# Performance work log

Hardware: AMD Instinct MI355X
Metric: run time of the kernel (lower is better)

## Reference

```python
import jax, jax.numpy as jnp
import numpy as np

NEG_INF = -1e30  # stand-in for float('-inf') added to masked scores


def setup_inputs() -> dict:
    key = jax.random.key(0)
    ks = jax.random.split(key, 3)
    B, S, D = 4, 2048, 1024
    x = jax.random.normal(ks[0], (B, S, D), dtype=jnp.float32)
    W_qkv = jax.random.normal(ks[1], (D, 3 * D), dtype=jnp.float32) * (1.0 / np.sqrt(D))
    b_qkv = jnp.zeros((3 * D,), dtype=jnp.float32)
    W_out = jax.random.normal(ks[2], (D, D), dtype=jnp.float32) * (1.0 / np.sqrt(D))
    b_out = jnp.zeros((D,), dtype=jnp.float32)
    return {"x": x, "W_qkv": W_qkv, "b_qkv": b_qkv, "W_out": W_out, "b_out": b_out, "mask": 1}


def reference(x, W_qkv, b_qkv, W_out, b_out, mask):
    B, S, D = x.shape
    H = 16
    hd = D // H
    # fused QKV projection: [B,S,3D]
    qkv = x @ W_qkv + b_qkv
    # [B,S,H,3*hd] -> [B,H,S,3*hd], split into q,k,v each [B,H,S,hd]
    qkv = qkv.reshape(B, S, H, 3 * hd).transpose(0, 2, 1, 3)
    q, k, v = jnp.split(qkv, 3, axis=-1)
    # scaled dot-product attention, full score matrix [B,H,S,S]
    scaled = jnp.einsum('bhqd,bhkd->bhqk', q, k) / np.sqrt(hd)
    if mask:
        causal = jnp.triu(jnp.ones((S, S), dtype=bool), k=1)
        scaled = jnp.where(causal, NEG_INF, scaled)
    attention = jax.nn.softmax(scaled, axis=-1)
    values = jnp.einsum('bhqk,bhkd->bhqd', attention, v)
    # merge heads: [B,H,S,hd] -> [B,S,D] (matches tf.reshape on [B,H,S,hd])
    values = values.reshape(B, S, H * hd)
    return values @ W_out + b_out
```

## Files before the change

### kernel.cpp

```cpp
#include <hip/hip_runtime.h>
#include <hip/hip_bf16.h>

typedef __attribute__((ext_vector_type(8))) short short8;
typedef __attribute__((ext_vector_type(4))) float f32x4;

__device__ inline f32x4 mfma16(short8 a, short8 b, f32x4 c) {
    return __builtin_amdgcn_mfma_f32_16x16x32_bf16(a, b, c, 0, 0, 0);
}
__device__ inline short f2bf(float x) {
    __hip_bfloat16 h = __float2bfloat16(x);
    return *reinterpret_cast<short*>(&h);
}
__device__ inline unsigned short f2bfu(float x) {
    __hip_bfloat16 h = __float2bfloat16(x);
    return *reinterpret_cast<unsigned short*>(&h);
}
__device__ inline float bf2f(short u) {
    __hip_bfloat16 h = *reinterpret_cast<__hip_bfloat16*>(&u);
    return __bfloat162float(h);
}
__device__ inline float scrub(float v, float s) {
    return (fabsf(v) < 1e30f) ? v : s;
}
__device__ inline short8 scaleq(short8 v) {
    short8 r;
#pragma unroll
    for (int j = 0; j < 8; j++) r[j] = f2bf(bf2f(v[j]) * 0.125f);
    return r;
}

__global__ void detect_dtype(const unsigned short* __restrict__ x, int* flag) {
    __shared__ int cnt;
    if (threadIdx.x == 0) cnt = 0;
    __syncthreads();
    int c = 0;
    for (int i = threadIdx.x; i < 1024; i += 256) {
        unsigned short u = x[i];
        int e = (u >> 7) & 0xFF;
        if ((u & 0x7FFF) == 0 || (e >= 110 && e <= 143)) c++;
    }
    atomicAdd(&cnt, c);
    __syncthreads();
    if (threadIdx.x == 0) flag[0] = (cnt < 819) ? 1 : 0;
}

__global__ void conv_bias(const void* __restrict__ in, short* __restrict__ out,
                          int n, const int* __restrict__ flag) {
    int i = blockIdx.x * 256 + threadIdx.x;
    if (i >= n) return;
    out[i] = (*flag) ? f2bf(((const float*)in)[i]) : ((const short*)in)[i];
}

__global__ __launch_bounds__(256) void conv_x(const void* __restrict__ in,
                                              short* __restrict__ out, int n,
                                              const int* __restrict__ flag) {
    int i = (blockIdx.x * 256 + threadIdx.x) * 4;
    if (i >= n) return;
    if (*flag) {
        float4 f = *(const float4*)((const float*)in + i);
        unsigned int u0 = ((unsigned int)f2bfu(f.y) << 16) | f2bfu(f.x);
        unsigned int u1 = ((unsigned int)f2bfu(f.w) << 16) | f2bfu(f.z);
        *(uint2*)(out + i) = make_uint2(u0, u1);
    } else {
        *(uint2*)(out + i) = *(const uint2*)((const short*)in + i);
    }
}

__global__ void fill_sentinel(void* out, int n, const int* __restrict__ flag) {
    int i = blockIdx.x * 256 + threadIdx.x;
    if (i >= n) return;
    if (*flag) ((float*)out)[i] = 3e5f; else ((short*)out)[i] = f2bf(3e5f);
}

__global__ __launch_bounds__(256) void transpose_poly(const void* __restrict__ in,
                                                      short* __restrict__ out,
                                                      int R, int C,
                                                      const int* __restrict__ flag) {
    __shared__ short tile[32][33];
    const bool f32 = (*flag) != 0;
    int tx = threadIdx.x & 31, ty = threadIdx.x >> 5;
    int r0 = blockIdx.y * 32, c0 = blockIdx.x * 32;
#pragma unroll
    for (int i = 0; i < 4; i++) {
        size_t off = (size_t)(r0 + ty + i * 8) * C + c0 + tx;
        tile[ty + i * 8][tx] = f32 ? f2bf(((const float*)in)[off]) : ((const short*)in)[off];
    }
    __syncthreads();
#pragma unroll
    for (int i = 0; i < 4; i++)
        out[(size_t)(c0 + ty + i * 8) * R + r0 + tx] = tile[tx][ty + i * 8];
}

#define LDK 72

__global__ __launch_bounds__(256) void gemm_bt(const short* __restrict__ A,
                                               const short* __restrict__ Bt,
                                               const short* __restrict__ bias,
                                               void* __restrict__ Cv,
                                               int N, int K,
                                               const int* __restrict__ flag,
                                               int c_poly, float sent) {
    alignas(16) __shared__ short As[128 * LDK];
    alignas(16) __shared__ short Bs[128 * LDK];
    const bool cf32 = c_poly && (*flag);
    int tid = threadIdx.x;
    int wave = tid >> 6, lane = tid & 63;
    int lrow = lane & 15, lq = lane >> 4;
    int wm = (wave >> 1) * 64, wn = (wave & 1) * 64;
    int m0 = blockIdx.y * 128, n0 = blockIdx.x * 128;

    f32x4 acc[4][4];
#pragma unroll
    for (int i = 0; i < 4; i++)
#pragma unroll
        for (int j = 0; j < 4; j++) acc[i][j] = (f32x4){0.f, 0.f, 0.f, 0.f};

    int srow = tid >> 3;
    int scol = (tid & 7) * 8;

    for (int kb = 0; kb < K; kb += 64) {
#pragma unroll
        for (int p = 0; p < 4; p++) {
            int row = p * 32 + srow;
            *(short8*)&As[row * LDK + scol] =
                *(const short8*)&A[(size_t)(m0 + row) * K + kb + scol];
            *(short8*)&Bs[row * LDK + scol] =
                *(const short8*)&Bt[(size_t)(n0 + row) * K + kb + scol];
        }
        __syncthreads();
#pragma unroll
        for (int ks = 0; ks < 2; ks++) {
            short8 af[4], bf[4];
#pragma unroll
            for (int i = 0; i < 4; i++)
                af[i] = *(short8*)&As[(wm + i * 16 + lrow) * LDK + ks * 32 + lq * 8];
#pragma unroll
            for (int i = 0; i < 4; i++)
                bf[i] = *(short8*)&Bs[(wn + i * 16 + lrow) * LDK + ks * 32 + lq * 8];
#pragma unroll
            for (int i = 0; i < 4; i++)
#pragma unroll
                for (int j = 0; j < 4; j++)
                    acc[i][j] = mfma16(af[i], bf[j], acc[i][j]);
        }
        __syncthreads();
    }

    const __hip_bfloat16* bias16 = (const __hip_bfloat16*)bias;
#pragma unroll
    for (int j = 0; j < 4; j++) {
        int col = n0 + wn + j * 16 + lrow;
        float bv = __bfloat162float(bias16[col]);
#pragma unroll
        for (int i = 0; i < 4; i++) {
            int rbase = m0 + wm + i * 16 + lq * 4;
#pragma unroll
            for (int r = 0; r < 4; r++) {
                float val = scrub(acc[i][j][r] + bv, sent);
                size_t off = (size_t)(rbase + r) * N + col;
                if (cf32) ((float*)Cv)[off] = val; else ((short*)Cv)[off] = f2bf(val);
            }
        }
    }
}

#define VP2 72
#define PP 72

__global__ __launch_bounds__(256) void attn_kernel(const short* __restrict__ QKV,
                                                   short* __restrict__ AO,
                                                   const int* __restrict__ maskp) {
    constexpr int S = 2048, C3 = 3072;
    alignas(16) __shared__ short Vt[2][64 * VP2];
    alignas(16) __shared__ short Pt[4][2][16 * PP];

    int tid = threadIdx.x;
    int wave = tid >> 6, lane = tid & 63;
    int lrow = lane & 15, lq = lane >> 4;
    int bh = blockIdx.y;
    const bool causal = (*maskp) != 0;
    const short* base = QKV + (size_t)(bh >> 4) * S * C3 + (bh & 15) * 192;

    int vi2 = (tid & 31) * 2;
    int vd0 = (tid >> 5) * 8;

    int buf = 0;
    for (int tile = 0; tile < 2; tile++) {
        int q0t = (tile == 0) ? blockIdx.x * 128 : 1920 - blockIdx.x * 128;

        int qg[2];
        short8 qf0[2], qf1[2];
#pragma unroll
        for (int g = 0; g < 2; g++) {
            qg[g] = q0t + wave * 32 + g * 16 + lrow;
            qf0[g] = scaleq(*(const short8*)(base + (size_t)qg[g] * C3 + lq * 8));
            qf1[g] = scaleq(*(const short8*)(base + (size_t)qg[g] * C3 + 32 + lq * 8));
        }

        float m_i[2] = {-1e38f, -1e38f}, l_i[2] = {0.f, 0.f};
        f32x4 acc[2][4];
#pragma unroll
        for (int g = 0; g < 2; g++)
#pragma unroll
            for (int nt = 0; nt < 4; nt++) acc[g][nt] = (f32x4){0.f, 0.f, 0.f, 0.f};

        int nkv = causal ? (q0t + 128) : S;

        for (int kv0 = 0; kv0 < nkv; kv0 += 64) {
            {
                const short* vs0 = base + (size_t)(kv0 + vi2) * C3 + 128 + vd0;
                union { short8 v; unsigned short u[8]; } a, b;
                a.v = *(const short8*)vs0;
                b.v = *(const short8*)(vs0 + C3);
                unsigned int* vt = (unsigned int*)&Vt[buf][0];
#pragma unroll
                for (int j = 0; j < 8; j++)
                    vt[((vd0 + j) * VP2 + vi2) >> 1] =
                        ((unsigned int)b.u[j] << 16) | a.u[j];
            }
            __syncthreads();

            f32x4 s[2][4];
#pragma unroll
            for (int sub = 0; sub < 4; sub++) {
                const short* kb = base + (size_t)(kv0 + sub * 16 + lrow) * C3 + 64;
                short8 kf0 = *(const short8*)(kb + lq * 8);
                short8 kf1 = *(const short8*)(kb + 32 + lq * 8);
#pragma unroll
                for (int g = 0; g < 2; g++) {
                    f32x4 a = (f32x4){0.f, 0.f, 0.f, 0.f};
                    a = mfma16(kf0, qf0[g], a);
                    a = mfma16(kf1, qf1[g], a);
                    s[g][sub] = a;
                }
            }

#pragma unroll
            for (int g = 0; g < 2; g++) {
                if (causal && (kv0 + 63 > q0t + wave * 32 + g * 16)) {
#pragma unroll
                    for (int sub = 0; sub < 4; sub++) {
                        int kvg = kv0 + sub * 16 + lq * 4;
#pragma unroll
                        for (int r = 0; r < 4; r++)
                            if (kvg + r > qg[g]) s[g][sub][r] = -1e30f;
                    }
                }
                float vmax = -1e38f;
#pragma unroll
                for (int sub = 0; sub < 4; sub++) {
                    float a = fmaxf(fmaxf(s[g][sub][0], s[g][sub][1]),
                                    fmaxf(s[g][sub][2], s[g][sub][3]));
                    vmax = fmaxf(vmax, a);
                }
                vmax = fmaxf(vmax, __shfl_xor(vmax, 16, 64));
                vmax = fmaxf(vmax, __shfl_xor(vmax, 32, 64));
                float mnew = fmaxf(m_i[g], vmax);
                float alpha = __expf(m_i[g] - mnew);
                float lsum = 0.f;
                unsigned int pk[4][2];
#pragma unroll
                for (int sub = 0; sub < 4; sub++) {
                    float p0 = __expf(s[g][sub][0] - mnew);
                    float p1 = __expf(s[g][sub][1] - mnew);
                    float p2 = __expf(s[g][sub][2] - mnew);
                    float p3 = __expf(s[g][sub][3] - mnew);
                    lsum += (p0 + p1) + (p2 + p3);
                    pk[sub][0] = ((unsigned int)f2bfu(p1) << 16) | f2bfu(p0);
                    pk[sub][1] = ((unsigned int)f2bfu(p3) << 16) | f2bfu(p2);
                }
                lsum += __shfl_xor(lsum, 16, 64);
                lsum += __shfl_xor(lsum, 32, 64);
                l_i[g] = l_i[g] * alpha + lsum;
                m_i[g] = mnew;
#pragma unroll
                for (int nt = 0; nt < 4; nt++)
#pragma unroll
                    for (int r = 0; r < 4; r++) acc[g][nt][r] *= alpha;
                unsigned int* pt = (unsigned int*)&Pt[wave][g][0];
#pragma unroll
                for (int sub = 0; sub < 4; sub++)
                    *(uint2*)&pt[(lrow * PP + sub * 16 + lq * 4) >> 1] =
                        make_uint2(pk[sub][0], pk[sub][1]);
            }

#pragma unroll
            for (int ks = 0; ks < 2; ks++) {
                short8 pfA = *(short8*)&Pt[wave][0][lrow * PP + ks * 32 + lq * 8];
                short8 pfB = *(short8*)&Pt[wave][1][lrow * PP + ks * 32 + lq * 8];
#pragma unroll
                for (int nt = 0; nt < 4; nt++) {
                    short8 vf = *(short8*)&Vt[buf][(nt * 16 + lrow) * VP2 + ks * 32 + lq * 8];
                    acc[0][nt] = mfma16(vf, pfA, acc[0][nt]);
                    acc[1][nt] = mfma16(vf, pfB, acc[1][nt]);
                }
            }
            buf ^= 1;
        }

#pragma unroll
        for (int g = 0; g < 2; g++) {
            float inv = 1.f / l_i[g];
            short* ob = AO + ((size_t)bh * S + qg[g]) * 64;
#pragma unroll
            for (int nt = 0; nt < 4; nt++) {
                unsigned int u0 = ((unsigned int)f2bfu(scrub(acc[g][nt][1] * inv, 4e4f)) << 16) |
                                  f2bfu(scrub(acc[g][nt][0] * inv, 4e4f));
                unsigned int u1 = ((unsigned int)f2bfu(scrub(acc[g][nt][3] * inv, 4e4f)) << 16) |
                                  f2bfu(scrub(acc[g][nt][2] * inv, 4e4f));
                *(uint2*)(ob + nt * 16 + lq * 4) = make_uint2(u0, u1);
            }
        }
    }
}

extern "C" void kernel_launch(void* const* d_in, const int* in_sizes, int n_in,
                              void* d_out, int out_size, void* d_ws, size_t ws_size,
                              hipStream_t stream) {
    char* ws = (char*)d_ws;
    int*   flag  = (int*)ws;
    short* bq_bf = (short*)(ws + 65536);
    short* bo_bf = (short*)(ws + 131072);
    short* WqkvT = (short*)(ws + (1ull << 20));
    short* WoutT = (short*)(ws + 7ull * (1ull << 20));
    short* xbfAO = (short*)(ws + 9ull * (1ull << 20));
    short* QKVc  = (short*)(ws + 25ull * (1ull << 20));

    detect_dtype<<<1, 256, 0, stream>>>((const unsigned short*)d_in[0], flag);

    if (ws_size < 73ull * 1048576) {
        fill_sentinel<<<(8388608 + 255) / 256, 256, 0, stream>>>(d_out, 8388608, flag);
        return;
    }

    conv_bias<<<12, 256, 0, stream>>>(d_in[2], bq_bf, 3072, flag);
    conv_bias<<<4, 256, 0, stream>>>(d_in[4], bo_bf, 1024, flag);
    transpose_poly<<<dim3(96, 32), 256, 0, stream>>>(d_in[1], WqkvT, 1024, 3072, flag);
    transpose_poly<<<dim3(32, 32), 256, 0, stream>>>(d_in[3], WoutT, 1024, 1024, flag);
    conv_x<<<8192, 256, 0, stream>>>(d_in[0], xbfAO, 8388608, flag);

    gemm_bt<<<dim3(24, 64), 256, 0, stream>>>(xbfAO, WqkvT, bq_bf, QKVc,
                                              3072, 1024, flag, 0, 8e4f);
    attn_kernel<<<dim3(8, 64), 256, 0, stream>>>(QKVc, xbfAO, (const int*)d_in[5]);
    gemm_bt<<<dim3(8, 64), 256, 0, stream>>>(xbfAO, WoutT, bo_bf, d_out,
                                             1024, 1024, flag, 1, 2e4f);
}
```

Before: 328.3 us.

## Split attention KV range across two wave groups and skip lazy rescaling

The attention block grows to 512 threads. Two groups of four waves each process alternating 64-wide KV chunks for the same query rows, and their partial softmax state (m, l, acc) is merged through shared memory at the end of each tile. This doubles the waves per block to raise parallelism and latency hiding, at the cost of extra LDS traffic and barriers. The online softmax also skips the max update and accumulator rescale when the new block max stays within 8 of the running max, which saves exp and multiply work but risks larger unnormalised exponents.

Result: slower. 388.4 us (+18.3%).

```diff
diff --git a/kernel.cpp b/kernel.cpp
--- a/kernel.cpp
+++ b/kernel.cpp
@@ -166,23 +166,29 @@
 
 #define VP2 72
 #define PP 72
-
-__global__ __launch_bounds__(256) void attn_kernel(const short* __restrict__ QKV,
-                                                   short* __restrict__ AO,
-                                                   const int* __restrict__ maskp) {
+#define VT_ELEMS (2 * 2 * 64 * VP2)
+#define PT_ELEMS (8 * 2 * 16 * PP)
+
+__global__ __launch_bounds__(512, 4) void attn_kernel(const short* __restrict__ QKV,
+                                                      short* __restrict__ AO,
+                                                      const int* __restrict__ maskp) {
     constexpr int S = 2048, C3 = 3072;
-    alignas(16) __shared__ short Vt[2][64 * VP2];
-    alignas(16) __shared__ short Pt[4][2][16 * PP];
+    alignas(16) __shared__ short smem[VT_ELEMS + PT_ELEMS];
 
     int tid = threadIdx.x;
     int wave = tid >> 6, lane = tid & 63;
+    int wq = wave & 3, gsel = wave >> 2;
     int lrow = lane & 15, lq = lane >> 4;
     int bh = blockIdx.y;
     const bool causal = (*maskp) != 0;
     const short* base = QKV + (size_t)(bh >> 4) * S * C3 + (bh & 15) * 192;
 
-    int vi2 = (tid & 31) * 2;
-    int vd0 = (tid >> 5) * 8;
+    int t8 = tid & 255;
+    int vi2 = (t8 & 31) * 2;
+    int vd0 = (t8 >> 5) * 8;
+
+    short* PtA = smem + VT_ELEMS + (wave * 2 + 0) * 16 * PP;
+    short* PtB = smem + VT_ELEMS + (wave * 2 + 1) * 16 * PP;
 
     int buf = 0;
     for (int tile = 0; tile < 2; tile++) {
@@ -192,7 +198,7 @@
         short8 qf0[2], qf1[2];
 #pragma unroll
         for (int g = 0; g < 2; g++) {
-            qg[g] = q0t + wave * 32 + g * 16 + lrow;
+            qg[g] = q0t + wq * 32 + g * 16 + lrow;
             qf0[g] = scaleq(*(const short8*)(base + (size_t)qg[g] * C3 + lq * 8));
             qf1[g] = scaleq(*(const short8*)(base + (size_t)qg[g] * C3 + 32 + lq * 8));
         }
@@ -206,13 +212,15 @@
 
         int nkv = causal ? (q0t + 128) : S;
 
-        for (int kv0 = 0; kv0 < nkv; kv0 += 64) {
+        for (int kv0g = 0; kv0g < nkv; kv0g += 128) {
+            int kv0 = kv0g + gsel * 64;
+            short* Vtc = smem + (gsel * 2 + buf) * 64 * VP2;
             {
                 const short* vs0 = base + (size_t)(kv0 + vi2) * C3 + 128 + vd0;
                 union { short8 v; unsigned short u[8]; } a, b;
                 a.v = *(const short8*)vs0;
                 b.v = *(const short8*)(vs0 + C3);
-                unsigned int* vt = (unsigned int*)&Vt[buf][0];
+                unsigned int* vt = (unsigned int*)Vtc;
 #pragma unroll
                 for (int j = 0; j < 8; j++)
                     vt[((vd0 + j) * VP2 + vi2) >> 1] =
@@ -237,7 +245,7 @@
 
 #pragma unroll
             for (int g = 0; g < 2; g++) {
-                if (causal && (kv0 + 63 > q0t + wave * 32 + g * 16)) {
+                if (causal && (kv0 + 63 > q0t + wq * 32 + g * 16)) {
 #pragma unroll
                     for (int sub = 0; sub < 4; sub++) {
                         int kvg = kv0 + sub * 16 + lq * 4;
@@ -255,8 +263,16 @@
                 }
                 vmax = fmaxf(vmax, __shfl_xor(vmax, 16, 64));
                 vmax = fmaxf(vmax, __shfl_xor(vmax, 32, 64));
-                float mnew = fmaxf(m_i[g], vmax);
-                float alpha = __expf(m_i[g] - mnew);
+                float mnew = m_i[g];
+                if (!__all(vmax <= m_i[g] + 8.0f)) {
+                    mnew = fmaxf(m_i[g], vmax);
+                    float alpha = __expf(m_i[g] - mnew);
+                    l_i[g] *= alpha;
+#pragma unroll
+                    for (int nt = 0; nt < 4; nt++)
+#pragma unroll
+                        for (int r = 0; r < 4; r++) acc[g][nt][r] *= alpha;
+                }
                 float lsum = 0.f;
                 unsigned int pk[4][2];
 #pragma unroll
@@ -271,13 +287,9 @@
                 }
                 lsum += __shfl_xor(lsum, 16, 64);
                 lsum += __shfl_xor(lsum, 32, 64);
-                l_i[g] = l_i[g] * alpha + lsum;
+                l_i[g] += lsum;
                 m_i[g] = mnew;
-#pragma unroll
-                for (int nt = 0; nt < 4; nt++)
-#pragma unroll
-                    for (int r = 0; r < 4; r++) acc[g][nt][r] *= alpha;
-                unsigned int* pt = (unsigned int*)&Pt[wave][g][0];
+                unsigned int* pt = (unsigned int*)(g ? PtB : PtA);
 #pragma unroll
                 for (int sub = 0; sub < 4; sub++)
                     *(uint2*)&pt[(lrow * PP + sub * 16 + lq * 4) >> 1] =
@@ -286,11 +298,11 @@
 
 #pragma unroll
             for (int ks = 0; ks < 2; ks++) {
-                short8 pfA = *(short8*)&Pt[wave][0][lrow * PP + ks * 32 + lq * 8];
-                short8 pfB = *(short8*)&Pt[wave][1][lrow * PP + ks * 32 + lq * 8];
+                short8 pfA = *(short8*)&PtA[lrow * PP + ks * 32 + lq * 8];
+                short8 pfB = *(short8*)&PtB[lrow * PP + ks * 32 + lq * 8];
 #pragma unroll
                 for (int nt = 0; nt < 4; nt++) {
-                    short8 vf = *(short8*)&Vt[buf][(nt * 16 + lrow) * VP2 + ks * 32 + lq * 8];
+                    short8 vf = *(short8*)&Vtc[(nt * 16 + lrow) * VP2 + ks * 32 + lq * 8];
                     acc[0][nt] = mfma16(vf, pfA, acc[0][nt]);
                     acc[1][nt] = mfma16(vf, pfB, acc[1][nt]);
                 }
@@ -298,19 +310,45 @@
             buf ^= 1;
         }
 
-#pragma unroll
-        for (int g = 0; g < 2; g++) {
-            float inv = 1.f / l_i[g];
-            short* ob = AO + ((size_t)bh * S + qg[g]) * 64;
-#pragma unroll
-            for (int nt = 0; nt < 4; nt++) {
-                unsigned int u0 = ((unsigned int)f2bfu(scrub(acc[g][nt][1] * inv, 4e4f)) << 16) |
-                                  f2bfu(scrub(acc[g][nt][0] * inv, 4e4f));
-                unsigned int u1 = ((unsigned int)f2bfu(scrub(acc[g][nt][3] * inv, 4e4f)) << 16) |
-                                  f2bfu(scrub(acc[g][nt][2] * inv, 4e4f));
-                *(uint2*)(ob + nt * 16 + lq * 4) = make_uint2(u0, u1);
-            }
-        }
+        __syncthreads();
+        float* ex = (float*)smem;
+        float* px = ex + (wq * 64 + lane) * 37;
+        if (gsel) {
+#pragma unroll
+            for (int g = 0; g < 2; g++) {
+                px[g * 18 + 0] = m_i[g];
+                px[g * 18 + 1] = l_i[g];
+#pragma unroll
+                for (int nt = 0; nt < 4; nt++)
+#pragma unroll
+                    for (int r = 0; r < 4; r++)
+                        px[g * 18 + 2 + nt * 4 + r] = acc[g][nt][r];
+            }
+        }
+        __syncthreads();
+        if (!gsel) {
+#pragma unroll
+            for (int g = 0; g < 2; g++) {
+                float mb = px[g * 18 + 0], lb = px[g * 18 + 1];
+                float mn = fmaxf(m_i[g], mb);
+                float ea = __expf(m_i[g] - mn), eb = __expf(mb - mn);
+                float inv = 1.f / (l_i[g] * ea + lb * eb);
+                float fa = ea * inv, fb = eb * inv;
+                short* ob = AO + ((size_t)bh * S + qg[g]) * 64;
+#pragma unroll
+                for (int nt = 0; nt < 4; nt++) {
+                    const float* pb = &px[g * 18 + 2 + nt * 4];
+                    float o0 = scrub(acc[g][nt][0] * fa + pb[0] * fb, 4e4f);
+                    float o1 = scrub(acc[g][nt][1] * fa + pb[1] * fb, 4e4f);
+                    float o2 = scrub(acc[g][nt][2] * fa + pb[2] * fb, 4e4f);
+                    float o3 = scrub(acc[g][nt][3] * fa + pb[3] * fb, 4e4f);
+                    unsigned int u0 = ((unsigned int)f2bfu(o1) << 16) | f2bfu(o0);
+                    unsigned int u1 = ((unsigned int)f2bfu(o3) << 16) | f2bfu(o2);
+                    *(uint2*)(ob + nt * 16 + lq * 4) = make_uint2(u0, u1);
+                }
+            }
+        }
+        __syncthreads();
     }
 }
 
@@ -341,7 +379,7 @@
 
     gemm_bt<<<dim3(24, 64), 256, 0, stream>>>(xbfAO, WqkvT, bq_bf, QKVc,
                                               3072, 1024, flag, 0, 8e4f);
-    attn_kernel<<<dim3(8, 64), 256, 0, stream>>>(QKVc, xbfAO, (const int*)d_in[5]);
+    attn_kernel<<<dim3(8, 64), 512, 0, stream>>>(QKVc, xbfAO, (const int*)d_in[5]);
     gemm_bt<<<dim3(8, 64), 256, 0, stream>>>(xbfAO, WoutT, bo_bf, d_out,
                                              1024, 1024, flag, 1, 2e4f);
 }
```

## Split paired causal query tiles into separate blocks with balanced 1D scheduling

Applied to the files above, without the earlier changes.

Each attention block used to process two query tiles (one early, one late) to balance causal work. Now each block handles one 128-row query tile, giving 1024 blocks, with a 1D grid whose index mapping interleaves heavy and light tiles across batch-heads. The aim is more parallelism and better load balance across CUs. The risk is extra per-block overhead and less predictable tail behaviour. The launch_bounds attribute is also removed, which may change how registers are allocated.

Result: slower. 370.5 us (+12.9%).

```diff
diff --git a/kernel.cpp b/kernel.cpp
--- a/kernel.cpp
+++ b/kernel.cpp
@@ -167,9 +167,9 @@
 #define VP2 72
 #define PP 72
 
-__global__ __launch_bounds__(256) void attn_kernel(const short* __restrict__ QKV,
-                                                   short* __restrict__ AO,
-                                                   const int* __restrict__ maskp) {
+__global__ void attn_kernel(const short* __restrict__ QKV,
+                            short* __restrict__ AO,
+                            const int* __restrict__ maskp) {
     constexpr int S = 2048, C3 = 3072;
     alignas(16) __shared__ short Vt[2][64 * VP2];
     alignas(16) __shared__ short Pt[4][2][16 * PP];
@@ -177,139 +177,146 @@
     int tid = threadIdx.x;
     int wave = tid >> 6, lane = tid & 63;
     int lrow = lane & 15, lq = lane >> 4;
-    int bh = blockIdx.y;
+
+    int id = blockIdx.x;
+    int u = id & 255, r = id >> 8;
+    int b = u & 15;
+    int bh = (u >> 4) + (r << 4);
+    int bxv;
+    if (r == 0)      bxv = b;
+    else if (r == 1) bxv = 15 - b;
+    else if (r == 2) bxv = (b + 8) & 15;
+    else             bxv = 15 - ((b + 8) & 15);
+    int q0t = bxv * 128;
+
     const bool causal = (*maskp) != 0;
     const short* base = QKV + (size_t)(bh >> 4) * S * C3 + (bh & 15) * 192;
 
     int vi2 = (tid & 31) * 2;
     int vd0 = (tid >> 5) * 8;
 
+    int qg[2];
+    short8 qf0[2], qf1[2];
+#pragma unroll
+    for (int g = 0; g < 2; g++) {
+        qg[g] = q0t + wave * 32 + g * 16 + lrow;
+        qf0[g] = scaleq(*(const short8*)(base + (size_t)qg[g] * C3 + lq * 8));
+        qf1[g] = scaleq(*(const short8*)(base + (size_t)qg[g] * C3 + 32 + lq * 8));
+    }
+
+    float m_i[2] = {-1e38f, -1e38f}, l_i[2] = {0.f, 0.f};
+    f32x4 acc[2][4];
+#pragma unroll
+    for (int g = 0; g < 2; g++)
+#pragma unroll
+        for (int nt = 0; nt < 4; nt++) acc[g][nt] = (f32x4){0.f, 0.f, 0.f, 0.f};
+
+    int nkv = causal ? (q0t + 128) : S;
+
     int buf = 0;
-    for (int tile = 0; tile < 2; tile++) {
-        int q0t = (tile == 0) ? blockIdx.x * 128 : 1920 - blockIdx.x * 128;
-
-        int qg[2];
-        short8 qf0[2], qf1[2];
+    for (int kv0 = 0; kv0 < nkv; kv0 += 64) {
+        {
+            const short* vs0 = base + (size_t)(kv0 + vi2) * C3 + 128 + vd0;
+            union { short8 v; unsigned short u[8]; } a, bb;
+            a.v = *(const short8*)vs0;
+            bb.v = *(const short8*)(vs0 + C3);
+            unsigned int* vt = (unsigned int*)&Vt[buf][0];
+#pragma unroll
+            for (int j = 0; j < 8; j++)
+                vt[((vd0 + j) * VP2 + vi2) >> 1] =
+                    ((unsigned int)bb.u[j] << 16) | a.u[j];
+        }
+        __syncthreads();
+
+        f32x4 s[2][4];
+#pragma unroll
+        for (int sub = 0; sub < 4; sub++) {
+            const short* kb = base + (size_t)(kv0 + sub * 16 + lrow) * C3 + 64;
+            short8 kf0 = *(const short8*)(kb + lq * 8);
+            short8 kf1 = *(const short8*)(kb + 32 + lq * 8);
+#pragma unroll
+            for (int g = 0; g < 2; g++) {
+                f32x4 a = (f32x4){0.f, 0.f, 0.f, 0.f};
+                a = mfma16(kf0, qf0[g], a);
+                a = mfma16(kf1, qf1[g], a);
+                s[g][sub] = a;
+            }
+        }
+
 #pragma unroll
         for (int g = 0; g < 2; g++) {
-            qg[g] = q0t + wave * 32 + g * 16 + lrow;
-            qf0[g] = scaleq(*(const short8*)(base + (size_t)qg[g] * C3 + lq * 8));
-            qf1[g] = scaleq(*(const short8*)(base + (size_t)qg[g] * C3 + 32 + lq * 8));
-        }
-
-        float m_i[2] = {-1e38f, -1e38f}, l_i[2] = {0.f, 0.f};
-        f32x4 acc[2][4];
-#pragma unroll
-        for (int g = 0; g < 2; g++)
-#pragma unroll
-            for (int nt = 0; nt < 4; nt++) acc[g][nt] = (f32x4){0.f, 0.f, 0.f, 0.f};
-
-        int nkv = causal ? (q0t + 128) : S;
-
-        for (int kv0 = 0; kv0 < nkv; kv0 += 64) {
-            {
-                const short* vs0 = base + (size_t)(kv0 + vi2) * C3 + 128 + vd0;
-                union { short8 v; unsigned short u[8]; } a, b;
-                a.v = *(const short8*)vs0;
-                b.v = *(const short8*)(vs0 + C3);
-                unsigned int* vt = (unsigned int*)&Vt[buf][0];
-#pragma unroll
-                for (int j = 0; j < 8; j++)
-                    vt[((vd0 + j) * VP2 + vi2) >> 1] =
-                        ((unsigned int)b.u[j] << 16) | a.u[j];
-            }
-            __syncthreads();
-
-            f32x4 s[2][4];
+            if (causal && (kv0 + 63 > q0t + wave * 32 + g * 16)) {
+#pragma unroll
+                for (int sub = 0; sub < 4; sub++) {
+                    int kvg = kv0 + sub * 16 + lq * 4;
+#pragma unroll
+                    for (int rr = 0; rr < 4; rr++)
+                        if (kvg + rr > qg[g]) s[g][sub][rr] = -1e30f;
+                }
+            }
+            float vmax = -1e38f;
 #pragma unroll
             for (int sub = 0; sub < 4; sub++) {
-                const short* kb = base + (size_t)(kv0 + sub * 16 + lrow) * C3 + 64;
-                short8 kf0 = *(const short8*)(kb + lq * 8);
-                short8 kf1 = *(const short8*)(kb + 32 + lq * 8);
-#pragma unroll
-                for (int g = 0; g < 2; g++) {
-                    f32x4 a = (f32x4){0.f, 0.f, 0.f, 0.f};
-                    a = mfma16(kf0, qf0[g], a);
-                    a = mfma16(kf1, qf1[g], a);
-                    s[g][sub] = a;
-                }
-            }
-
-#pragma unroll
-            for (int g = 0; g < 2; g++) {
-                if (causal && (kv0 + 63 > q0t + wave * 32 + g * 16)) {
-#pragma unroll
-                    for (int sub = 0; sub < 4; sub++) {
-                        int kvg = kv0 + sub * 16 + lq * 4;
-#pragma unroll
-                        for (int r = 0; r < 4; r++)
-                            if (kvg + r > qg[g]) s[g][sub][r] = -1e30f;
-                    }
-                }
-                float vmax = -1e38f;
-#pragma unroll
-                for (int sub = 0; sub < 4; sub++) {
-                    float a = fmaxf(fmaxf(s[g][sub][0], s[g][sub][1]),
-                                    fmaxf(s[g][sub][2], s[g][sub][3]));
-                    vmax = fmaxf(vmax, a);
-                }
-                vmax = fmaxf(vmax, __shfl_xor(vmax, 16, 64));
-                vmax = fmaxf(vmax, __shfl_xor(vmax, 32, 64));
-                float mnew = fmaxf(m_i[g], vmax);
-                float alpha = __expf(m_i[g] - mnew);
-                float lsum = 0.f;
-                unsigned int pk[4][2];
-#pragma unroll
-                for (int sub = 0; sub < 4; sub++) {
-                    float p0 = __expf(s[g][sub][0] - mnew);
-                    float p1 = __expf(s[g][sub][1] - mnew);
-                    float p2 = __expf(s[g][sub][2] - mnew);
-                    float p3 = __expf(s[g][sub][3] - mnew);
-                    lsum += (p0 + p1) + (p2 + p3);
-                    pk[sub][0] = ((unsigned int)f2bfu(p1) << 16) | f2bfu(p0);
-                    pk[sub][1] = ((unsigned int)f2bfu(p3) << 16) | f2bfu(p2);
-                }
-                lsum += __shfl_xor(lsum, 16, 64);
-                lsum += __shfl_xor(lsum, 32, 64);
-                l_i[g] = l_i[g] * alpha + lsum;
-                m_i[g] = mnew;
-#pragma unroll
-                for (int nt = 0; nt < 4; nt++)
-#pragma unroll
-                    for (int r = 0; r < 4; r++) acc[g][nt][r] *= alpha;
-                unsigned int* pt = (unsigned int*)&Pt[wave][g][0];
-#pragma unroll
-                for (int sub = 0; sub < 4; sub++)
-                    *(uint2*)&pt[(lrow * PP + sub * 16 + lq * 4) >> 1] =
-                        make_uint2(pk[sub][0], pk[sub][1]);
-            }
-
-#pragma unroll
-            for (int ks = 0; ks < 2; ks++) {
-                short8 pfA = *(short8*)&Pt[wave][0][lrow * PP + ks * 32 + lq * 8];
-                short8 pfB = *(short8*)&Pt[wave][1][lrow * PP + ks * 32 + lq * 8];
-#pragma unroll
-                for (int nt = 0; nt < 4; nt++) {
-                    short8 vf = *(short8*)&Vt[buf][(nt * 16 + lrow) * VP2 + ks * 32 + lq * 8];
-                    acc[0][nt] = mfma16(vf, pfA, acc[0][nt]);
-                    acc[1][nt] = mfma16(vf, pfB, acc[1][nt]);
-                }
-            }
-            buf ^= 1;
-        }
-
-#pragma unroll
-        for (int g = 0; g < 2; g++) {
-            float inv = 1.f / l_i[g];
-            short* ob = AO + ((size_t)bh * S + qg[g]) * 64;
+                float a = fmaxf(fmaxf(s[g][sub][0], s[g][sub][1]),
+                                fmaxf(s[g][sub][2], s[g][sub][3]));
+                vmax = fmaxf(vmax, a);
+            }
+            vmax = fmaxf(vmax, __shfl_xor(vmax, 16, 64));
+            vmax = fmaxf(vmax, __shfl_xor(vmax, 32, 64));
+            float mnew = fmaxf(m_i[g], vmax);
+            float alpha = __expf(m_i[g] - mnew);
+            float lsum = 0.f;
+            unsigned int pk[4][2];
+#pragma unroll
+            for (int sub = 0; sub < 4; sub++) {
+                float p0 = __expf(s[g][sub][0] - mnew);
+                float p1 = __expf(s[g][sub][1] - mnew);
+                float p2 = __expf(s[g][sub][2] - mnew);
+                float p3 = __expf(s[g][sub][3] - mnew);
+                lsum += (p0 + p1) + (p2 + p3);
+                pk[sub][0] = ((unsigned int)f2bfu(p1) << 16) | f2bfu(p0);
+                pk[sub][1] = ((unsigned int)f2bfu(p3) << 16) | f2bfu(p2);
+            }
+            lsum += __shfl_xor(lsum, 16, 64);
+            lsum += __shfl_xor(lsum, 32, 64);
+            l_i[g] = l_i[g] * alpha + lsum;
+            m_i[g] = mnew;
+#pragma unroll
+            for (int nt = 0; nt < 4; nt++)
+#pragma unroll
+                for (int rr = 0; rr < 4; rr++) acc[g][nt][rr] *= alpha;
+            unsigned int* pt = (unsigned int*)&Pt[wave][g][0];
+#pragma unroll
+            for (int sub = 0; sub < 4; sub++)
+                *(uint2*)&pt[(lrow * PP + sub * 16 + lq * 4) >> 1] =
+                    make_uint2(pk[sub][0], pk[sub][1]);
+        }
+
+#pragma unroll
+        for (int ks = 0; ks < 2; ks++) {
+            short8 pfA = *(short8*)&Pt[wave][0][lrow * PP + ks * 32 + lq * 8];
+            short8 pfB = *(short8*)&Pt[wave][1][lrow * PP + ks * 32 + lq * 8];
 #pragma unroll
             for (int nt = 0; nt < 4; nt++) {
-                unsigned int u0 = ((unsigned int)f2bfu(scrub(acc[g][nt][1] * inv, 4e4f)) << 16) |
-                                  f2bfu(scrub(acc[g][nt][0] * inv, 4e4f));
-                unsigned int u1 = ((unsigned int)f2bfu(scrub(acc[g][nt][3] * inv, 4e4f)) << 16) |
-                                  f2bfu(scrub(acc[g][nt][2] * inv, 4e4f));
-                *(uint2*)(ob + nt * 16 + lq * 4) = make_uint2(u0, u1);
-            }
+                short8 vf = *(short8*)&Vt[buf][(nt * 16 + lrow) * VP2 + ks * 32 + lq * 8];
+                acc[0][nt] = mfma16(vf, pfA, acc[0][nt]);
+                acc[1][nt] = mfma16(vf, pfB, acc[1][nt]);
+            }
+        }
+        buf ^= 1;
+    }
+
+#pragma unroll
+    for (int g = 0; g < 2; g++) {
+        float inv = 1.f / l_i[g];
+        short* ob = AO + ((size_t)bh * S + qg[g]) * 64;
+#pragma unroll
+        for (int nt = 0; nt < 4; nt++) {
+            unsigned int u0 = ((unsigned int)f2bfu(scrub(acc[g][nt][1] * inv, 4e4f)) << 16) |
+                              f2bfu(scrub(acc[g][nt][0] * inv, 4e4f));
+            unsigned int u1 = ((unsigned int)f2bfu(scrub(acc[g][nt][3] * inv, 4e4f)) << 16) |
+                              f2bfu(scrub(acc[g][nt][2] * inv, 4e4f));
+            *(uint2*)(ob + nt * 16 + lq * 4) = make_uint2(u0, u1);
         }
     }
 }
@@ -341,7 +348,7 @@
 
     gemm_bt<<<dim3(24, 64), 256, 0, stream>>>(xbfAO, WqkvT, bq_bf, QKVc,
                                               3072, 1024, flag, 0, 8e4f);
-    attn_kernel<<<dim3(8, 64), 256, 0, stream>>>(QKVc, xbfAO, (const int*)d_in[5]);
+    attn_kernel<<<dim3(1024), 256, 0, stream>>>(QKVc, xbfAO, (const int*)d_in[5]);
     gemm_bt<<<dim3(8, 64), 256, 0, stream>>>(xbfAO, WoutT, bo_bf, d_out,
                                              1024, 1024, flag, 1, 2e4f);
 }
```

## Shrink attention query tile to 64 rows per block, doubling grid

Applied to the files above, without the earlier changes.

Each wave now handles one 16-row query group instead of two, so a block covers 64 query rows and the attention grid doubles to 16x64 blocks. Causal pairing of tiles is kept, now pairing tile i with 31-i. The aim is more blocks for better occupancy and load balance across CUs, with fewer registers per thread. In exchange, each K/V tile loaded into LDS and registers serves only half as many queries, which doubles K/V traffic per query. A barrier is also added at the end of each tile.

Result: slower. 433.5 us (+32.1%).

```diff
diff --git a/kernel.cpp b/kernel.cpp
--- a/kernel.cpp
+++ b/kernel.cpp
@@ -172,7 +172,7 @@
                                                    const int* __restrict__ maskp) {
     constexpr int S = 2048, C3 = 3072;
     alignas(16) __shared__ short Vt[2][64 * VP2];
-    alignas(16) __shared__ short Pt[4][2][16 * PP];
+    alignas(16) __shared__ short Pt[4][16 * PP];
 
     int tid = threadIdx.x;
     int wave = tid >> 6, lane = tid & 63;
@@ -186,131 +186,116 @@
 
     int buf = 0;
     for (int tile = 0; tile < 2; tile++) {
-        int q0t = (tile == 0) ? blockIdx.x * 128 : 1920 - blockIdx.x * 128;
-
-        int qg[2];
-        short8 qf0[2], qf1[2];
-#pragma unroll
-        for (int g = 0; g < 2; g++) {
-            qg[g] = q0t + wave * 32 + g * 16 + lrow;
-            qf0[g] = scaleq(*(const short8*)(base + (size_t)qg[g] * C3 + lq * 8));
-            qf1[g] = scaleq(*(const short8*)(base + (size_t)qg[g] * C3 + 32 + lq * 8));
-        }
-
-        float m_i[2] = {-1e38f, -1e38f}, l_i[2] = {0.f, 0.f};
-        f32x4 acc[2][4];
-#pragma unroll
-        for (int g = 0; g < 2; g++)
-#pragma unroll
-            for (int nt = 0; nt < 4; nt++) acc[g][nt] = (f32x4){0.f, 0.f, 0.f, 0.f};
-
-        int nkv = causal ? (q0t + 128) : S;
+        int q0t = (tile == 0) ? blockIdx.x * 64 : (31 - blockIdx.x) * 64;
+
+        int qg = q0t + wave * 16 + lrow;
+        short8 qf0 = scaleq(*(const short8*)(base + (size_t)qg * C3 + lq * 8));
+        short8 qf1 = scaleq(*(const short8*)(base + (size_t)qg * C3 + 32 + lq * 8));
+
+        float m_i = -1e38f, l_i = 0.f;
+        f32x4 acc[4];
+#pragma unroll
+        for (int nt = 0; nt < 4; nt++) acc[nt] = (f32x4){0.f, 0.f, 0.f, 0.f};
+
+        int nkv = causal ? (q0t + 64) : S;
 
         for (int kv0 = 0; kv0 < nkv; kv0 += 64) {
             {
                 const short* vs0 = base + (size_t)(kv0 + vi2) * C3 + 128 + vd0;
-                union { short8 v; unsigned short u[8]; } a, b;
+                union { short8 v; unsigned short u[8]; } a, bb;
                 a.v = *(const short8*)vs0;
-                b.v = *(const short8*)(vs0 + C3);
+                bb.v = *(const short8*)(vs0 + C3);
                 unsigned int* vt = (unsigned int*)&Vt[buf][0];
 #pragma unroll
                 for (int j = 0; j < 8; j++)
                     vt[((vd0 + j) * VP2 + vi2) >> 1] =
-                        ((unsigned int)b.u[j] << 16) | a.u[j];
+                        ((unsigned int)bb.u[j] << 16) | a.u[j];
             }
             __syncthreads();
 
-            f32x4 s[2][4];
+            f32x4 s[4];
 #pragma unroll
             for (int sub = 0; sub < 4; sub++) {
                 const short* kb = base + (size_t)(kv0 + sub * 16 + lrow) * C3 + 64;
                 short8 kf0 = *(const short8*)(kb + lq * 8);
                 short8 kf1 = *(const short8*)(kb + 32 + lq * 8);
-#pragma unroll
-                for (int g = 0; g < 2; g++) {
-                    f32x4 a = (f32x4){0.f, 0.f, 0.f, 0.f};
-                    a = mfma16(kf0, qf0[g], a);
-                    a = mfma16(kf1, qf1[g], a);
-                    s[g][sub] = a;
+                f32x4 a = (f32x4){0.f, 0.f, 0.f, 0.f};
+                a = mfma16(kf0, qf0, a);
+                a = mfma16(kf1, qf1, a);
+                s[sub] = a;
+            }
+
+            if (causal && (kv0 + 63 > q0t + wave * 16)) {
+#pragma unroll
+                for (int sub = 0; sub < 4; sub++) {
+                    int kvg = kv0 + sub * 16 + lq * 4;
+#pragma unroll
+                    for (int rr = 0; rr < 4; rr++)
+                        if (kvg + rr > qg) s[sub][rr] = -1e30f;
                 }
             }
-
-#pragma unroll
-            for (int g = 0; g < 2; g++) {
-                if (causal && (kv0 + 63 > q0t + wave * 32 + g * 16)) {
-#pragma unroll
-                    for (int sub = 0; sub < 4; sub++) {
-                        int kvg = kv0 + sub * 16 + lq * 4;
-#pragma unroll
-                        for (int r = 0; r < 4; r++)
-                            if (kvg + r > qg[g]) s[g][sub][r] = -1e30f;
-                    }
-                }
-                float vmax = -1e38f;
-#pragma unroll
-                for (int sub = 0; sub < 4; sub++) {
-                    float a = fmaxf(fmaxf(s[g][sub][0], s[g][sub][1]),
-                                    fmaxf(s[g][sub][2], s[g][sub][3]));
-                    vmax = fmaxf(vmax, a);
-                }
-                vmax = fmaxf(vmax, __shfl_xor(vmax, 16, 64));
-                vmax = fmaxf(vmax, __shfl_xor(vmax, 32, 64));
-                float mnew = fmaxf(m_i[g], vmax);
-                float alpha = __expf(m_i[g] - mnew);
-                float lsum = 0.f;
-                unsigned int pk[4][2];
-#pragma unroll
-                for (int sub = 0; sub < 4; sub++) {
-                    float p0 = __expf(s[g][sub][0] - mnew);
-                    float p1 = __expf(s[g][sub][1] - mnew);
-                    float p2 = __expf(s[g][sub][2] - mnew);
-                    float p3 = __expf(s[g][sub][3] - mnew);
-                    lsum += (p0 + p1) + (p2 + p3);
-                    pk[sub][0] = ((unsigned int)f2bfu(p1) << 16) | f2bfu(p0);
-                    pk[sub][1] = ((unsigned int)f2bfu(p3) << 16) | f2bfu(p2);
-                }
-                lsum += __shfl_xor(lsum, 16, 64);
-                lsum += __shfl_xor(lsum, 32, 64);
-                l_i[g] = l_i[g] * alpha + lsum;
-                m_i[g] = mnew;
-#pragma unroll
-                for (int nt = 0; nt < 4; nt++)
-#pragma unroll
-                    for (int r = 0; r < 4; r++) acc[g][nt][r] *= alpha;
-                unsigned int* pt = (unsigned int*)&Pt[wave][g][0];
-#pragma unroll
-                for (int sub = 0; sub < 4; sub++)
-                    *(uint2*)&pt[(lrow * PP + sub * 16 + lq * 4) >> 1] =
-                        make_uint2(pk[sub][0], pk[sub][1]);
-            }
+            float vmax = -1e38f;
+#pragma unroll
+            for (int sub = 0; sub < 4; sub++) {
+                float a = fmaxf(fmaxf(s[sub][0], s[sub][1]),
+                                fmaxf(s[sub][2], s[sub][3]));
+                vmax = fmaxf(vmax, a);
+            }
+            vmax = fmaxf(vmax, __shfl_xor(vmax, 16, 64));
+            vmax = fmaxf(vmax, __shfl_xor(vmax, 32, 64));
+            float mnew = fmaxf(m_i, vmax);
+            float alpha = __expf(m_i - mnew);
+            float lsum = 0.f;
+            unsigned int pk[4][2];
+#pragma unroll
+            for (int sub = 0; sub < 4; sub++) {
+                float p0 = __expf(s[sub][0] - mnew);
+                float p1 = __expf(s[sub][1] - mnew);
+                float p2 = __expf(s[sub][2] - mnew);
+                float p3 = __expf(s[sub][3] - mnew);
+                lsum += (p0 + p1) + (p2 + p3);
+                pk[sub][0] = ((unsigned int)f2bfu(p1) << 16) | f2bfu(p0);
+                pk[sub][1] = ((unsigned int)f2bfu(p3) << 16) | f2bfu(p2);
+            }
+            lsum += __shfl_xor(lsum, 16, 64);
+            lsum += __shfl_xor(lsum, 32, 64);
+            l_i = l_i * alpha + lsum;
+            m_i = mnew;
+#pragma unroll
+            for (int nt = 0; nt < 4; nt++)
+#pragma unroll
+                for (int rr = 0; rr < 4; rr++) acc[nt][rr] *= alpha;
+            unsigned int* pt = (unsigned int*)&Pt[wave][0];
+#pragma unroll
+            for (int sub = 0; sub < 4; sub++)
+                *(uint2*)&pt[(lrow * PP + sub * 16 + lq * 4) >> 1] =
+                    make_uint2(pk[sub][0], pk[sub][1]);
 
 #pragma unroll
             for (int ks = 0; ks < 2; ks++) {
-                short8 pfA = *(short8*)&Pt[wave][0][lrow * PP + ks * 32 + lq * 8];
-                short8 pfB = *(short8*)&Pt[wave][1][lrow * PP + ks * 32 + lq * 8];
+                short8 pf = *(short8*)&Pt[wave][lrow * PP + ks * 32 + lq * 8];
 #pragma unroll
                 for (int nt = 0; nt < 4; nt++) {
                     short8 vf = *(short8*)&Vt[buf][(nt * 16 + lrow) * VP2 + ks * 32 + lq * 8];
-                    acc[0][nt] = mfma16(vf, pfA, acc[0][nt]);
-                    acc[1][nt] = mfma16(vf, pfB, acc[1][nt]);
+                    acc[nt] = mfma16(vf, pf, acc[nt]);
                 }
             }
             buf ^= 1;
         }
 
-#pragma unroll
-        for (int g = 0; g < 2; g++) {
-            float inv = 1.f / l_i[g];
-            short* ob = AO + ((size_t)bh * S + qg[g]) * 64;
+        {
+            float inv = 1.f / l_i;
+            short* ob = AO + ((size_t)bh * S + qg) * 64;
 #pragma unroll
             for (int nt = 0; nt < 4; nt++) {
-                unsigned int u0 = ((unsigned int)f2bfu(scrub(acc[g][nt][1] * inv, 4e4f)) << 16) |
-                                  f2bfu(scrub(acc[g][nt][0] * inv, 4e4f));
-                unsigned int u1 = ((unsigned int)f2bfu(scrub(acc[g][nt][3] * inv, 4e4f)) << 16) |
-                                  f2bfu(scrub(acc[g][nt][2] * inv, 4e4f));
+                unsigned int u0 = ((unsigned int)f2bfu(scrub(acc[nt][1] * inv, 4e4f)) << 16) |
+                                  f2bfu(scrub(acc[nt][0] * inv, 4e4f));
+                unsigned int u1 = ((unsigned int)f2bfu(scrub(acc[nt][3] * inv, 4e4f)) << 16) |
+                                  f2bfu(scrub(acc[nt][2] * inv, 4e4f));
                 *(uint2*)(ob + nt * 16 + lq * 4) = make_uint2(u0, u1);
             }
         }
+        __syncthreads();
     }
 }
 
@@ -341,7 +326,7 @@
 
     gemm_bt<<<dim3(24, 64), 256, 0, stream>>>(xbfAO, WqkvT, bq_bf, QKVc,
                                               3072, 1024, flag, 0, 8e4f);
-    attn_kernel<<<dim3(8, 64), 256, 0, stream>>>(QKVc, xbfAO, (const int*)d_in[5]);
+    attn_kernel<<<dim3(16, 64), 256, 0, stream>>>(QKVc, xbfAO, (const int*)d_in[5]);
     gemm_bt<<<dim3(8, 64), 256, 0, stream>>>(xbfAO, WoutT, bo_bf, d_out,
                                              1024, 1024, flag, 1, 2e4f);
 }
```
